# Performance work log

Measured on AMD Instinct MI355X. Metric: run time of the kernel, lower is better.

The kernel has to match this reference:

```python
import jax, jax.numpy as jnp
import numpy as np

DIM = 1024
NUM_HEADS = 16
HEAD_DIM = DIM // NUM_HEADS
TAU = 1.0
LAMBDA_JUMP = 0.6
LAMBDA_LOCAL = 0.4
MIN_ENTROPY = 0.5
WINDOW = 3
EPS = 1e-10


def local_diffusion_kernel(seq_len, strength, window=WINDOW):
    # Banded Gaussian kernel, row-normalized. [S, S]
    i = jnp.arange(seq_len)
    d = i[:, None] - i[None, :]
    k = jnp.where(jnp.abs(d) <= window,
                  jnp.exp(-(d.astype(jnp.float32) ** 2) / (2.0 * strength ** 2)),
                  0.0)
    return k / (k.sum(axis=-1, keepdims=True) + EPS)


def setup_inputs() -> dict:
    key = jax.random.key(0)
    ks = jax.random.split(key, 9)
    scale = 0.02
    x = jax.random.normal(ks[0], (2, 2048, DIM), dtype=jnp.float32)
    Wq = jax.random.normal(ks[1], (DIM, DIM), dtype=jnp.float32) * scale
    bq = jax.random.normal(ks[2], (DIM,), dtype=jnp.float32) * scale
    Wk = jax.random.normal(ks[3], (DIM, DIM), dtype=jnp.float32) * scale
    bk = jax.random.normal(ks[4], (DIM,), dtype=jnp.float32) * scale
    Wv = jax.random.normal(ks[5], (DIM, DIM), dtype=jnp.float32) * scale
    bv = jax.random.normal(ks[6], (DIM,), dtype=jnp.float32) * scale
    Wo = jax.random.normal(ks[7], (DIM, DIM), dtype=jnp.float32) * scale
    bo = jax.random.normal(ks[8], (DIM,), dtype=jnp.float32) * scale
    return {"x": x, "Wq": Wq, "bq": bq, "Wk": Wk, "bk": bk,
            "Wv": Wv, "bv": bv, "Wo": Wo, "bo": bo}


def reference(x, Wq, bq, Wk, bk, Wv, bv, Wo, bo):
    B, S, D = x.shape
    H, hd = NUM_HEADS, HEAD_DIM
    # torch Linear: y = x @ W.T + b
    Q = (x @ Wq.T + bq).reshape(B, S, H, hd).transpose(0, 2, 1, 3)  # [B,H,S,hd]
    K = (x @ Wk.T + bk).reshape(B, S, H, hd).transpose(0, 2, 1, 3)
    V = (x @ Wv.T + bv).reshape(B, S, H, hd).transpose(0, 2, 1, 3)

    scores = jnp.einsum('bhqd,bhkd->bhqk', Q, K) / (TAU * np.sqrt(hd).astype(np.float32))
    A = jax.nn.softmax(scores, axis=-1)  # [B,H,S,S]

    # Per-row entropy gating (detach-based in torch: forward value is unchanged)
    entropy = -jnp.sum(A * jnp.log(A + EPS), axis=-1, keepdims=True)
    stable = jax.lax.stop_gradient((entropy >= MIN_ENTROPY).astype(A.dtype))
    A = stable * A + (1.0 - stable) * jax.lax.stop_gradient(A)

    L = local_diffusion_kernel(S, LAMBDA_LOCAL)  # [S,S]
    A_stable = LAMBDA_JUMP * A + (1.0 - LAMBDA_JUMP) * L[None, None, :, :]

    out = jnp.einsum('bhqk,bhkd->bhqd', A_stable, V)  # [B,H,S,hd]
    out = out.transpose(0, 2, 1, 3).reshape(B, S, D)
    return out @ Wo.T + bo
```

## Files before the change

### kernel.cpp

```cpp
#include <hip/hip_runtime.h>
#include <math.h>

typedef __bf16 bf16x8 __attribute__((ext_vector_type(8)));
typedef float f32x4 __attribute__((ext_vector_type(4)));

namespace {
constexpr int DIMC = 1024, NH = 16, HD = 64, SEQ = 2048;
constexpr float SCL2 = 0.1803368801f;
}

__device__ __forceinline__ unsigned short f2b(float f) {
  unsigned u = __float_as_uint(f);
  return (unsigned short)((u + 0x7fffu + ((u >> 16) & 1u)) >> 16);
}
__device__ __forceinline__ float b2f(unsigned short s) {
  return __uint_as_float((unsigned)s << 16);
}
__device__ __forceinline__ unsigned cvtpk(float lo, float hi) {
  unsigned r;
  asm("v_cvt_pk_bf16_f32 %0, %1, %2" : "=v"(r) : "v"(lo), "v"(hi));
  return r;
}
__device__ __forceinline__ void gld16(void* l, const void* g) {
  __builtin_amdgcn_global_load_lds(
      (const __attribute__((address_space(1))) void*)g,
      (__attribute__((address_space(3))) void*)l, 16, 0, 0);
}

__global__ __launch_bounds__(256)
void cvt_bf16(const float* __restrict__ in, unsigned short* __restrict__ out, int n8) {
  int i = blockIdx.x * 256 + threadIdx.x;
  if (i >= n8) return;
  const float4* in4 = (const float4*)in;
  float4 a = in4[2 * i], b = in4[2 * i + 1];
  union { unsigned short u[8]; uint4 v; } r;
  r.u[0] = f2b(a.x); r.u[1] = f2b(a.y); r.u[2] = f2b(a.z); r.u[3] = f2b(a.w);
  r.u[4] = f2b(b.x); r.u[5] = f2b(b.y); r.u[6] = f2b(b.z); r.u[7] = f2b(b.w);
  ((uint4*)out)[i] = r.v;
}

__global__ __launch_bounds__(256)
void cvt_w4(const float* __restrict__ w0, const float* __restrict__ w1,
            const float* __restrict__ w2, const float* __restrict__ w3,
            unsigned short* __restrict__ out) {
  const int which = blockIdx.y;
  const float* src = which == 0 ? w0 : which == 1 ? w1 : which == 2 ? w2 : w3;
  unsigned short* dst = out + (size_t)which * 1048576;
  int i = blockIdx.x * 256 + threadIdx.x;
  const float4* in4 = (const float4*)src;
  float4 a = in4[2 * i], b = in4[2 * i + 1];
  union { unsigned short u[8]; uint4 v; } r;
  r.u[0] = f2b(a.x); r.u[1] = f2b(a.y); r.u[2] = f2b(a.z); r.u[3] = f2b(a.w);
  r.u[4] = f2b(b.x); r.u[5] = f2b(b.y); r.u[6] = f2b(b.z); r.u[7] = f2b(b.w);
  ((uint4*)dst)[i] = r.v;
}

template<int MODE>
__device__ __forceinline__
void gemm_tile128(const unsigned short* __restrict__ A, const unsigned short* __restrict__ W,
                  const float* __restrict__ bias, void* __restrict__ Cout,
                  int bm, int bn, float scl, char* As, char* Bs) {
  const int tid = threadIdx.x, lane = tid & 63, w = tid >> 6;
  const int p = lane & 15, g = lane >> 4;
  const int wr = w >> 1, wc = w & 1;
  const int sr = tid >> 2, sc = (tid & 3) * 8;

  f32x4 acc[4][4];
#pragma unroll
  for (int mf = 0; mf < 4; ++mf)
#pragma unroll
    for (int nf = 0; nf < 4; ++nf)
      acc[mf][nf] = (f32x4){0.f, 0.f, 0.f, 0.f};

  const size_t arow0 = (size_t)(bm + sr) * DIMC + sc;
  const size_t arow1 = (size_t)(bm + 64 + sr) * DIMC + sc;
  const size_t brow0 = (size_t)(bn + sr) * DIMC + sc;
  const size_t brow1 = (size_t)(bn + 64 + sr) * DIMC + sc;

  for (int k0 = 0; k0 < DIMC; k0 += 32) {
    __syncthreads();
    gld16(&As[tid * 16],        &A[arow0 + k0]);
    gld16(&As[4096 + tid * 16], &A[arow1 + k0]);
    gld16(&Bs[tid * 16],        &W[brow0 + k0]);
    gld16(&Bs[4096 + tid * 16], &W[brow1 + k0]);
    __syncthreads();
    bf16x8 af[4], bfr[4];
#pragma unroll
    for (int mf = 0; mf < 4; ++mf)
      af[mf] = *(const bf16x8*)&As[(wr * 64 + mf * 16 + p) * 64 + g * 16];
#pragma unroll
    for (int nf = 0; nf < 4; ++nf)
      bfr[nf] = *(const bf16x8*)&Bs[(wc * 64 + nf * 16 + p) * 64 + g * 16];
#pragma unroll
    for (int mf = 0; mf < 4; ++mf)
#pragma unroll
      for (int nf = 0; nf < 4; ++nf)
        acc[mf][nf] = __builtin_amdgcn_mfma_f32_16x16x32_bf16(af[mf], bfr[nf], acc[mf][nf], 0, 0, 0);
  }

#pragma unroll
  for (int nf = 0; nf < 4; ++nf) {
    const int cg = bn + wc * 64 + nf * 16 + p;
    const float bv = bias[cg & (DIMC - 1)];
#pragma unroll
    for (int mf = 0; mf < 4; ++mf) {
#pragma unroll
      for (int j = 0; j < 4; ++j) {
        const int rg = bm + wr * 64 + mf * 16 + g * 4 + j;
        const float v = (acc[mf][nf][j] + bv) * scl;
        if (MODE == 0) {
          ((float*)Cout)[(size_t)rg * DIMC + cg] = v;
        } else {
          const int bb = rg >> 11, ss = rg & (SEQ - 1);
          const int hh = cg >> 6, dd = cg & (HD - 1);
          ((unsigned short*)Cout)[(((size_t)(bb * NH + hh) * SEQ + ss) * HD) + dd] = f2b(v);
        }
      }
    }
  }
}

__global__ __launch_bounds__(256, 2)
void gemm_qkv(const unsigned short* __restrict__ A, const unsigned short* __restrict__ Wall,
              const float* __restrict__ bq, const float* __restrict__ bk,
              const float* __restrict__ bv, unsigned short* __restrict__ Out) {
  __shared__ char As[8192];
  __shared__ char Bs[8192];
  const int which = blockIdx.z;
  const unsigned short* W = Wall + (size_t)which * 1048576;
  const float* bias = which == 0 ? bq : which == 1 ? bk : bv;
  unsigned short* Cout = Out + (size_t)which * 4194304;
  const float scl = which == 0 ? SCL2 : 1.0f;
  gemm_tile128<1>(A, W, bias, Cout, blockIdx.x * 128, blockIdx.y * 128, scl, As, Bs);
}

__global__ __launch_bounds__(256, 2)
void gemm_out(const unsigned short* __restrict__ A, const unsigned short* __restrict__ W,
              const float* __restrict__ bias, float* __restrict__ Cout) {
  __shared__ char As[8192];
  __shared__ char Bs[4096];
  const int tid = threadIdx.x, lane = tid & 63, w = tid >> 6;
  const int p = lane & 15, g = lane >> 4;
  const int wr = w >> 1, wc = w & 1;
  const int bm = blockIdx.x * 128, bn = blockIdx.y * 64;
  const int sr = tid >> 2, sc = (tid & 3) * 8;

  f32x4 acc[4][2];
#pragma unroll
  for (int mf = 0; mf < 4; ++mf)
#pragma unroll
    for (int nf = 0; nf < 2; ++nf)
      acc[mf][nf] = (f32x4){0.f, 0.f, 0.f, 0.f};

  const size_t arow0 = (size_t)(bm + sr) * DIMC + sc;
  const size_t arow1 = (size_t)(bm + 64 + sr) * DIMC + sc;
  const size_t brow  = (size_t)(bn + sr) * DIMC + sc;

  for (int k0 = 0; k0 < DIMC; k0 += 32) {
    __syncthreads();
    gld16(&As[tid * 16],        &A[arow0 + k0]);
    gld16(&As[4096 + tid * 16], &A[arow1 + k0]);
    gld16(&Bs[tid * 16],        &W[brow + k0]);
    __syncthreads();
    bf16x8 af[4], bfr[2];
#pragma unroll
    for (int mf = 0; mf < 4; ++mf)
      af[mf] = *(const bf16x8*)&As[(wr * 64 + mf * 16 + p) * 64 + g * 16];
#pragma unroll
    for (int nf = 0; nf < 2; ++nf)
      bfr[nf] = *(const bf16x8*)&Bs[(wc * 32 + nf * 16 + p) * 64 + g * 16];
#pragma unroll
    for (int mf = 0; mf < 4; ++mf)
#pragma unroll
      for (int nf = 0; nf < 2; ++nf)
        acc[mf][nf] = __builtin_amdgcn_mfma_f32_16x16x32_bf16(af[mf], bfr[nf], acc[mf][nf], 0, 0, 0);
  }

#pragma unroll
  for (int nf = 0; nf < 2; ++nf) {
    const int cg = bn + wc * 32 + nf * 16 + p;
    const float bv = bias[cg];
#pragma unroll
    for (int mf = 0; mf < 4; ++mf) {
#pragma unroll
      for (int j = 0; j < 4; ++j) {
        const int rg = bm + wr * 64 + mf * 16 + g * 4 + j;
        Cout[(size_t)rg * DIMC + cg] = acc[mf][nf][j] + bv;
      }
    }
  }
}

__global__ __launch_bounds__(256, 2)
void attn_fused(const unsigned short* __restrict__ Q, const unsigned short* __restrict__ K,
                const unsigned short* __restrict__ V, unsigned short* __restrict__ Y) {
  __shared__ char Vt[2][8192];
  __shared__ char Pl[2][16384];
  const int tid = threadIdx.x, lane = tid & 63, w = tid >> 6;
  const int p = lane & 15, g = lane >> 4;
  const int bh = blockIdx.x, b = bh >> 4, h = bh & 15;
  const int q0 = blockIdx.y * 128, qw = q0 + w * 32;
  const size_t base = (size_t)bh * SEQ * HD;
  const unsigned short* Qp = Q + base;
  const unsigned short* Kp = K + base;
  const unsigned short* Vp = V + base;

  union Vu { bf16x8 v; unsigned short u[8]; };

  bf16x8 qf[2][2];
#pragma unroll
  for (int mi = 0; mi < 2; ++mi)
#pragma unroll
    for (int ks = 0; ks < 2; ++ks)
      qf[mi][ks] = *(const bf16x8*)&Qp[(size_t)(qw + mi * 16 + p) * HD + ks * 32 + g * 8];

  bf16x8 ones8;
  {
    union { unsigned short u[8]; bf16x8 v; } o;
#pragma unroll
    for (int e = 0; e < 8; ++e) o.u[e] = (p == 0) ? (unsigned short)0x3F80 : (unsigned short)0;
    ones8 = o.v;
  }

  f32x4 o2[2][4];
  f32x4 ol[2];
#pragma unroll
  for (int mi = 0; mi < 2; ++mi) {
#pragma unroll
    for (int nf = 0; nf < 4; ++nf)
      o2[mi][nf] = (f32x4){0.f, 0.f, 0.f, 0.f};
    ol[mi] = (f32x4){0.f, 0.f, 0.f, 0.f};
  }

  const int kp = tid & 31, vd0 = (tid >> 5) * 8;

  bf16x8 kf[4][2];
  Vu v0, v1;
  f32x4 s2[2][4];
  unsigned pk[2][8];

  auto loadK = [&](int kb) {
#pragma unroll
    for (int nf = 0; nf < 4; ++nf)
#pragma unroll
      for (int ks = 0; ks < 2; ++ks)
        kf[nf][ks] = *(const bf16x8*)&Kp[(size_t)(kb + nf * 16 + p) * HD + ks * 32 + g * 8];
  };
  auto loadV = [&](int kb) {
    v0.v = *(const bf16x8*)&Vp[(size_t)(kb + 2 * kp) * HD + vd0];
    v1.v = *(const bf16x8*)&Vp[(size_t)(kb + 2 * kp + 1) * HD + vd0];
  };
  auto qkt = [&]() {
#pragma unroll
    for (int mi = 0; mi < 2; ++mi)
#pragma unroll
      for (int nf = 0; nf < 4; ++nf)
        s2[mi][nf] = (f32x4){0.f, 0.f, 0.f, 0.f};
    __builtin_amdgcn_s_setprio(1);
#pragma unroll
    for (int mi = 0; mi < 2; ++mi)
#pragma unroll
      for (int nf = 0; nf < 4; ++nf)
#pragma unroll
        for (int ks = 0; ks < 2; ++ks)
          s2[mi][nf] = __builtin_amdgcn_mfma_f32_16x16x32_bf16(kf[nf][ks], qf[mi][ks], s2[mi][nf], 0, 0, 0);
    __builtin_amdgcn_s_setprio(0);
  };
  auto softmax = [&]() {
#pragma unroll
    for (int mi = 0; mi < 2; ++mi) {
#pragma unroll
      for (int nf = 0; nf < 4; ++nf)
#pragma unroll
        for (int j = 0; j < 4; ++j)
          s2[mi][nf][j] = exp2f(s2[mi][nf][j]);
#pragma unroll
      for (int nf = 0; nf < 4; ++nf) {
        pk[mi][2 * nf]     = cvtpk(s2[mi][nf][0], s2[mi][nf][1]);
        pk[mi][2 * nf + 1] = cvtpk(s2[mi][nf][2], s2[mi][nf][3]);
      }
    }
  };
  auto stage = [&](int par) {
#pragma unroll
    for (int mi = 0; mi < 2; ++mi) {
      const int r = w * 32 + mi * 16 + p;
      const int swz = (r & 7) << 4;
#pragma unroll
      for (int nf = 0; nf < 4; ++nf) {
        uint2 val; val.x = pk[mi][2 * nf]; val.y = pk[mi][2 * nf + 1];
        *(uint2*)&Pl[par][r * 128 + ((nf * 32 + g * 8) ^ swz)] = val;
      }
    }
#pragma unroll
    for (int e = 0; e < 8; ++e) {
      const int d = vd0 + e;
      const unsigned val = (unsigned)v0.u[e] | ((unsigned)v1.u[e] << 16);
      *(unsigned*)&Vt[par][d * 128 + ((kp * 4) ^ ((d & 7) << 4))] = val;
    }
  };
  auto pv = [&](int par) {
    bf16x8 pf[2][2], vb[4][2];
#pragma unroll
    for (int mi = 0; mi < 2; ++mi) {
      const int r = w * 32 + mi * 16 + p;
      const int swz = (r & 7) << 4;
#pragma unroll
      for (int ks = 0; ks < 2; ++ks)
        pf[mi][ks] = *(const bf16x8*)&Pl[par][r * 128 + ((ks * 64 + g * 16) ^ swz)];
    }
#pragma unroll
    for (int nfd = 0; nfd < 4; ++nfd) {
      const int d = nfd * 16 + p;
      const int swz = (d & 7) << 4;
#pragma unroll
      for (int ks = 0; ks < 2; ++ks)
        vb[nfd][ks] = *(const bf16x8*)&Vt[par][d * 128 + ((ks * 64 + g * 16) ^ swz)];
    }
    __builtin_amdgcn_s_setprio(1);
#pragma unroll
    for (int mi = 0; mi < 2; ++mi)
#pragma unroll
      for (int nfd = 0; nfd < 4; ++nfd)
#pragma unroll
        for (int ks = 0; ks < 2; ++ks)
          o2[mi][nfd] = __builtin_amdgcn_mfma_f32_16x16x32_bf16(vb[nfd][ks], pf[mi][ks], o2[mi][nfd], 0, 0, 0);
#pragma unroll
    for (int mi = 0; mi < 2; ++mi)
#pragma unroll
      for (int ks = 0; ks < 2; ++ks)
        ol[mi] = __builtin_amdgcn_mfma_f32_16x16x32_bf16(ones8, pf[mi][ks], ol[mi], 0, 0, 0);
    __builtin_amdgcn_s_setprio(0);
  };

  loadK(0);
  loadV(0);
  qkt();
  softmax();
  stage(0);
  __syncthreads();

  for (int kt = 1; kt < SEQ / 64; ++kt) {
    const int kb = kt * 64;
    loadK(kb);
    loadV(kb);
    pv((kt - 1) & 1);
    qkt();
    softmax();
    stage(kt & 1);
    __syncthreads();
  }
  pv(1);

  const float e1 = 4.3936934e-2f, e2 = 3.7266532e-6f, e3 = 6.1019804e-13f;
  const float lwv[4] = {1.f, e1, e2, e3};
#pragma unroll
  for (int mi = 0; mi < 2; ++mi) {
    const int q = qw + mi * 16 + p;
    const float lq = __shfl(ol[mi][0], p);
    const float inv = 0.6f / lq;
    float wsum = 0.f;
#pragma unroll
    for (int dd = -3; dd <= 3; ++dd) {
      const int kk = q + dd;
      if (kk >= 0 && kk < SEQ) wsum += lwv[dd < 0 ? -dd : dd];
    }
    const float wn = 0.4f / (wsum + 1e-10f);
#pragma unroll
    for (int nfd = 0; nfd < 4; ++nfd) {
      const int d0 = nfd * 16 + g * 4;
      float loc[4] = {0.f, 0.f, 0.f, 0.f};
#pragma unroll
      for (int dd = -3; dd <= 3; ++dd) {
        const int kk = q + dd;
        if (kk >= 0 && kk < SEQ) {
          const uint2 lv = *(const uint2*)&Vp[(size_t)kk * HD + d0];
          const float wt = lwv[dd < 0 ? -dd : dd];
          loc[0] = fmaf(wt, b2f((unsigned short)lv.x), loc[0]);
          loc[1] = fmaf(wt, b2f((unsigned short)(lv.x >> 16)), loc[1]);
          loc[2] = fmaf(wt, b2f((unsigned short)lv.y), loc[2]);
          loc[3] = fmaf(wt, b2f((unsigned short)(lv.y >> 16)), loc[3]);
        }
      }
      uint2 st;
      st.x = cvtpk(o2[mi][nfd][0] * inv + loc[0] * wn, o2[mi][nfd][1] * inv + loc[1] * wn);
      st.y = cvtpk(o2[mi][nfd][2] * inv + loc[2] * wn, o2[mi][nfd][3] * inv + loc[3] * wn);
      *(uint2*)&Y[((size_t)(b * SEQ + q)) * DIMC + h * HD + d0] = st;
    }
  }
}

extern "C" void kernel_launch(void* const* d_in, const int* in_sizes, int n_in,
                              void* d_out, int out_size, void* d_ws, size_t ws_size,
                              hipStream_t stream) {
  (void)in_sizes; (void)n_in; (void)out_size; (void)ws_size;
  const float* x  = (const float*)d_in[0];
  const float* Wq = (const float*)d_in[1];
  const float* bq = (const float*)d_in[2];
  const float* Wk = (const float*)d_in[3];
  const float* bk = (const float*)d_in[4];
  const float* Wv = (const float*)d_in[5];
  const float* bv = (const float*)d_in[6];
  const float* Wo = (const float*)d_in[7];
  const float* bo = (const float*)d_in[8];

  char* ws = (char*)d_ws;
  unsigned short* xb  = (unsigned short*)(ws);
  unsigned short* Wqb = (unsigned short*)(ws + 8388608);
  unsigned short* Wob = (unsigned short*)(ws + 14680064);
  unsigned short* Qh  = (unsigned short*)(ws + 16777216);
  unsigned short* Kh  = (unsigned short*)(ws + 25165824);
  unsigned short* Vh  = (unsigned short*)(ws + 33554432);
  unsigned short* Yb  = (unsigned short*)(ws + 41943040);

  dim3 blk(256);
  cvt_bf16<<<2048, blk, 0, stream>>>(x, xb, 524288);
  cvt_w4<<<dim3(512, 4), blk, 0, stream>>>(Wq, Wk, Wv, Wo, Wqb);

  gemm_qkv<<<dim3(32, 8, 3), blk, 0, stream>>>(xb, Wqb, bq, bk, bv, Qh);

  attn_fused<<<dim3(32, 16), blk, 0, stream>>>(Qh, Kh, Vh, Yb);

  gemm_out<<<dim3(32, 16), blk, 0, stream>>>(Yb, Wob, bo, (float*)d_out);
}
```

Before: 151.7 us.

## Split key range across wave pairs with private LDS and final reduction

Each wave now handles 64 query rows over half of the key sequence, and wave pairs split the 2048 keys. Each wave gets its own LDS region for P and transposed V, so the per-iteration block-wide __syncthreads is removed. The partial outputs and row sums are merged once through LDS at the end. In exchange, LDS use grows to 72KB, register pressure rises with larger accumulators, K and Q reuse per wave changes, and half the waves sit idle during the epilogue.

Measured after the change: 148.2 us. -2.4%, faster.

```diff
diff --git a/kernel.cpp b/kernel.cpp
--- a/kernel.cpp
+++ b/kernel.cpp
@@ -194,25 +194,29 @@
 __global__ __launch_bounds__(256, 2)
 void attn_fused(const unsigned short* __restrict__ Q, const unsigned short* __restrict__ K,
                 const unsigned short* __restrict__ V, unsigned short* __restrict__ Y) {
-  __shared__ char Vt[2][8192];
-  __shared__ char Pl[2][16384];
+  __shared__ char lds[73728];
   const int tid = threadIdx.x, lane = tid & 63, w = tid >> 6;
   const int p = lane & 15, g = lane >> 4;
   const int bh = blockIdx.x, b = bh >> 4, h = bh & 15;
-  const int q0 = blockIdx.y * 128, qw = q0 + w * 32;
+  const int q0 = blockIdx.y * 128;
+  const int qg = w & 1, kst = w >> 1;
+  const int qwv = q0 + qg * 64;
   const size_t base = (size_t)bh * SEQ * HD;
   const unsigned short* Qp = Q + base;
   const unsigned short* Kp = K + base;
   const unsigned short* Vp = V + base;
 
+  char* myPl = lds + w * 16384;
+  char* myVt = lds + w * 16384 + 8192;
+
   union Vu { bf16x8 v; unsigned short u[8]; };
 
-  bf16x8 qf[2][2];
-#pragma unroll
-  for (int mi = 0; mi < 2; ++mi)
+  bf16x8 qf[4][2];
+#pragma unroll
+  for (int mi = 0; mi < 4; ++mi)
 #pragma unroll
     for (int ks = 0; ks < 2; ++ks)
-      qf[mi][ks] = *(const bf16x8*)&Qp[(size_t)(qw + mi * 16 + p) * HD + ks * 32 + g * 8];
+      qf[mi][ks] = *(const bf16x8*)&Qp[(size_t)(qwv + mi * 16 + p) * HD + ks * 32 + g * 8];
 
   bf16x8 ones8;
   {
@@ -222,141 +226,151 @@
     ones8 = o.v;
   }
 
-  f32x4 o2[2][4];
-  f32x4 ol[2];
-#pragma unroll
-  for (int mi = 0; mi < 2; ++mi) {
+  const int kp = lane & 31, dgrp = lane >> 5;
+  const unsigned short* kA = Kp + (size_t)kst * 1024 * HD + (size_t)p * HD + g * 8;
+  const unsigned short* vP = Vp + (size_t)kst * 1024 * HD + (size_t)(2 * kp) * HD + dgrp * 8;
+
+  const int swz = (p & 7) << 4;
+  int pwCol[4], sCol[2], colE[8];
+#pragma unroll
+  for (int nf = 0; nf < 4; ++nf) pwCol[nf] = (nf * 32 + g * 8) ^ swz;
+#pragma unroll
+  for (int ks = 0; ks < 2; ++ks) sCol[ks] = (ks * 64 + g * 16) ^ swz;
+#pragma unroll
+  for (int e = 0; e < 8; ++e) colE[e] = (kp * 4) ^ (e << 4);
+  char* vtD = myVt + dgrp * 1024;
+
+  f32x4 o2[4][4];
+  f32x4 ol[4];
+#pragma unroll
+  for (int mi = 0; mi < 4; ++mi) {
 #pragma unroll
     for (int nf = 0; nf < 4; ++nf)
       o2[mi][nf] = (f32x4){0.f, 0.f, 0.f, 0.f};
     ol[mi] = (f32x4){0.f, 0.f, 0.f, 0.f};
   }
 
-  const int kp = tid & 31, vd0 = (tid >> 5) * 8;
-
   bf16x8 kf[4][2];
-  Vu v0, v1;
-  f32x4 s2[2][4];
-  unsigned pk[2][8];
-
-  auto loadK = [&](int kb) {
-#pragma unroll
-    for (int nf = 0; nf < 4; ++nf)
+  Vu vv[4][2];
+
+  auto loadKV = [&]() {
+    kf[0][0] = *(const bf16x8*)(kA + 0);    kf[0][1] = *(const bf16x8*)(kA + 32);
+    kf[1][0] = *(const bf16x8*)(kA + 1024); kf[1][1] = *(const bf16x8*)(kA + 1056);
+    kf[2][0] = *(const bf16x8*)(kA + 2048); kf[2][1] = *(const bf16x8*)(kA + 2080);
+    kf[3][0] = *(const bf16x8*)(kA + 3072); kf[3][1] = *(const bf16x8*)(kA + 3104);
+#pragma unroll
+    for (int c = 0; c < 4; ++c) {
+      vv[c][0].v = *(const bf16x8*)(vP + c * 16);
+      vv[c][1].v = *(const bf16x8*)(vP + HD + c * 16);
+    }
+    kA += 4096; vP += 4096;
+  };
+  auto scoreStage = [&]() {
+#pragma unroll
+    for (int mi = 0; mi < 4; ++mi) {
+      f32x4 s[4];
+#pragma unroll
+      for (int nf = 0; nf < 4; ++nf) s[nf] = (f32x4){0.f, 0.f, 0.f, 0.f};
+      __builtin_amdgcn_s_setprio(1);
+#pragma unroll
+      for (int nf = 0; nf < 4; ++nf)
+#pragma unroll
+        for (int ks = 0; ks < 2; ++ks)
+          s[nf] = __builtin_amdgcn_mfma_f32_16x16x32_bf16(kf[nf][ks], qf[mi][ks], s[nf], 0, 0, 0);
+      __builtin_amdgcn_s_setprio(0);
+#pragma unroll
+      for (int nf = 0; nf < 4; ++nf)
+#pragma unroll
+        for (int j = 0; j < 4; ++j)
+          s[nf][j] = exp2f(s[nf][j]);
+#pragma unroll
+      for (int nf = 0; nf < 4; ++nf) {
+        uint2 val;
+        val.x = cvtpk(s[nf][0], s[nf][1]);
+        val.y = cvtpk(s[nf][2], s[nf][3]);
+        *(uint2*)(myPl + p * 128 + mi * 2048 + pwCol[nf]) = val;
+      }
+    }
+  };
+  auto stageVt = [&]() {
+#pragma unroll
+    for (int c = 0; c < 4; ++c)
+#pragma unroll
+      for (int e = 0; e < 8; ++e) {
+        const unsigned val = (unsigned)vv[c][0].u[e] | ((unsigned)vv[c][1].u[e] << 16);
+        *(unsigned*)(vtD + c * 2048 + e * 128 + colE[e]) = val;
+      }
+  };
+  auto pv = [&]() {
+    bf16x8 vb[4][2];
+#pragma unroll
+    for (int nfd = 0; nfd < 4; ++nfd)
 #pragma unroll
       for (int ks = 0; ks < 2; ++ks)
-        kf[nf][ks] = *(const bf16x8*)&Kp[(size_t)(kb + nf * 16 + p) * HD + ks * 32 + g * 8];
+        vb[nfd][ks] = *(const bf16x8*)(myVt + p * 128 + nfd * 2048 + sCol[ks]);
+#pragma unroll
+    for (int mi = 0; mi < 4; ++mi) {
+      bf16x8 pf[2];
+#pragma unroll
+      for (int ks = 0; ks < 2; ++ks)
+        pf[ks] = *(const bf16x8*)(myPl + p * 128 + mi * 2048 + sCol[ks]);
+      __builtin_amdgcn_s_setprio(1);
+#pragma unroll
+      for (int nfd = 0; nfd < 4; ++nfd)
+#pragma unroll
+        for (int ks = 0; ks < 2; ++ks)
+          o2[mi][nfd] = __builtin_amdgcn_mfma_f32_16x16x32_bf16(vb[nfd][ks], pf[ks], o2[mi][nfd], 0, 0, 0);
+#pragma unroll
+      for (int ks = 0; ks < 2; ++ks)
+        ol[mi] = __builtin_amdgcn_mfma_f32_16x16x32_bf16(ones8, pf[ks], ol[mi], 0, 0, 0);
+      __builtin_amdgcn_s_setprio(0);
+    }
   };
-  auto loadV = [&](int kb) {
-    v0.v = *(const bf16x8*)&Vp[(size_t)(kb + 2 * kp) * HD + vd0];
-    v1.v = *(const bf16x8*)&Vp[(size_t)(kb + 2 * kp + 1) * HD + vd0];
-  };
-  auto qkt = [&]() {
-#pragma unroll
-    for (int mi = 0; mi < 2; ++mi)
-#pragma unroll
-      for (int nf = 0; nf < 4; ++nf)
-        s2[mi][nf] = (f32x4){0.f, 0.f, 0.f, 0.f};
-    __builtin_amdgcn_s_setprio(1);
-#pragma unroll
-    for (int mi = 0; mi < 2; ++mi)
-#pragma unroll
-      for (int nf = 0; nf < 4; ++nf)
-#pragma unroll
-        for (int ks = 0; ks < 2; ++ks)
-          s2[mi][nf] = __builtin_amdgcn_mfma_f32_16x16x32_bf16(kf[nf][ks], qf[mi][ks], s2[mi][nf], 0, 0, 0);
-    __builtin_amdgcn_s_setprio(0);
-  };
-  auto softmax = [&]() {
-#pragma unroll
-    for (int mi = 0; mi < 2; ++mi) {
-#pragma unroll
-      for (int nf = 0; nf < 4; ++nf)
-#pragma unroll
-        for (int j = 0; j < 4; ++j)
-          s2[mi][nf][j] = exp2f(s2[mi][nf][j]);
-#pragma unroll
-      for (int nf = 0; nf < 4; ++nf) {
-        pk[mi][2 * nf]     = cvtpk(s2[mi][nf][0], s2[mi][nf][1]);
-        pk[mi][2 * nf + 1] = cvtpk(s2[mi][nf][2], s2[mi][nf][3]);
-      }
-    }
-  };
-  auto stage = [&](int par) {
-#pragma unroll
-    for (int mi = 0; mi < 2; ++mi) {
-      const int r = w * 32 + mi * 16 + p;
-      const int swz = (r & 7) << 4;
-#pragma unroll
-      for (int nf = 0; nf < 4; ++nf) {
-        uint2 val; val.x = pk[mi][2 * nf]; val.y = pk[mi][2 * nf + 1];
-        *(uint2*)&Pl[par][r * 128 + ((nf * 32 + g * 8) ^ swz)] = val;
-      }
-    }
-#pragma unroll
-    for (int e = 0; e < 8; ++e) {
-      const int d = vd0 + e;
-      const unsigned val = (unsigned)v0.u[e] | ((unsigned)v1.u[e] << 16);
-      *(unsigned*)&Vt[par][d * 128 + ((kp * 4) ^ ((d & 7) << 4))] = val;
-    }
-  };
-  auto pv = [&](int par) {
-    bf16x8 pf[2][2], vb[4][2];
-#pragma unroll
-    for (int mi = 0; mi < 2; ++mi) {
-      const int r = w * 32 + mi * 16 + p;
-      const int swz = (r & 7) << 4;
-#pragma unroll
-      for (int ks = 0; ks < 2; ++ks)
-        pf[mi][ks] = *(const bf16x8*)&Pl[par][r * 128 + ((ks * 64 + g * 16) ^ swz)];
-    }
-#pragma unroll
-    for (int nfd = 0; nfd < 4; ++nfd) {
-      const int d = nfd * 16 + p;
-      const int swz = (d & 7) << 4;
-#pragma unroll
-      for (int ks = 0; ks < 2; ++ks)
-        vb[nfd][ks] = *(const bf16x8*)&Vt[par][d * 128 + ((ks * 64 + g * 16) ^ swz)];
-    }
-    __builtin_amdgcn_s_setprio(1);
-#pragma unroll
-    for (int mi = 0; mi < 2; ++mi)
+
+  loadKV();
+  scoreStage();
+  stageVt();
+  for (int kt = 1; kt < 16; ++kt) {
+    loadKV();
+    pv();
+    scoreStage();
+    stageVt();
+  }
+  pv();
+
+  if (kst == 1) {
+    char* dst = lds + w * 16384;
+#pragma unroll
+    for (int mi = 0; mi < 4; ++mi)
 #pragma unroll
       for (int nfd = 0; nfd < 4; ++nfd)
-#pragma unroll
-        for (int ks = 0; ks < 2; ++ks)
-          o2[mi][nfd] = __builtin_amdgcn_mfma_f32_16x16x32_bf16(vb[nfd][ks], pf[mi][ks], o2[mi][nfd], 0, 0, 0);
-#pragma unroll
-    for (int mi = 0; mi < 2; ++mi)
-#pragma unroll
-      for (int ks = 0; ks < 2; ++ks)
-        ol[mi] = __builtin_amdgcn_mfma_f32_16x16x32_bf16(ones8, pf[mi][ks], ol[mi], 0, 0, 0);
-    __builtin_amdgcn_s_setprio(0);
-  };
-
-  loadK(0);
-  loadV(0);
-  qkt();
-  softmax();
-  stage(0);
+        *(f32x4*)(dst + (mi * 4 + nfd) * 1024 + lane * 16) = o2[mi][nfd];
+    char* dsl = lds + 65536 + (w - 2) * 4096;
+#pragma unroll
+    for (int mi = 0; mi < 4; ++mi)
+      *(f32x4*)(dsl + mi * 1024 + lane * 16) = ol[mi];
+  }
   __syncthreads();
-
-  for (int kt = 1; kt < SEQ / 64; ++kt) {
-    const int kb = kt * 64;
-    loadK(kb);
-    loadV(kb);
-    pv((kt - 1) & 1);
-    qkt();
-    softmax();
-    stage(kt & 1);
-    __syncthreads();
-  }
-  pv(1);
+  if (kst == 1) return;
+
+  {
+    const char* src = lds + (w + 2) * 16384;
+#pragma unroll
+    for (int mi = 0; mi < 4; ++mi)
+#pragma unroll
+      for (int nfd = 0; nfd < 4; ++nfd)
+        o2[mi][nfd] += *(const f32x4*)(src + (mi * 4 + nfd) * 1024 + lane * 16);
+    const char* sl = lds + 65536 + w * 4096;
+#pragma unroll
+    for (int mi = 0; mi < 4; ++mi)
+      ol[mi] += *(const f32x4*)(sl + mi * 1024 + lane * 16);
+  }
 
   const float e1 = 4.3936934e-2f, e2 = 3.7266532e-6f, e3 = 6.1019804e-13f;
   const float lwv[4] = {1.f, e1, e2, e3};
 #pragma unroll
-  for (int mi = 0; mi < 2; ++mi) {
-    const int q = qw + mi * 16 + p;
+  for (int mi = 0; mi < 4; ++mi) {
+    const int q = qwv + mi * 16 + p;
     const float lq = __shfl(ol[mi][0], p);
     const float inv = 0.6f / lq;
     float wsum = 0.f;
```
